# Optimization experiments

Measured on AMD Instinct MI355X. Metric: run time of the kernel, lower is better.

The kernel has to match this reference:

```python
import jax, jax.numpy as jnp
import numpy as np

B, N, C, H = 2, 2048, 768, 12
D = C // H
SCALE = D ** -0.5
STEP = 0.1
LAMBD = 0.5
EPS = 1e-12  # F.normalize eps


def setup_inputs() -> dict:
    key = jax.random.key(0)
    k1, k2, k3 = jax.random.split(key, 3)
    x = jax.random.normal(k1, (B, N, C), dtype=jnp.float32)
    Wqkv = jax.random.normal(k2, (3 * C, C), dtype=jnp.float32) * 0.02
    Wproj = jax.random.normal(k3, (C, C), dtype=jnp.float32) * 0.02
    bproj = jnp.zeros((C,), dtype=jnp.float32)
    return {"x": x, "Wqkv": Wqkv, "Wproj": Wproj, "bproj": bproj}


def _l2_normalize(t):
    # matches F.normalize(t, dim=-1): t / max(||t||_2, eps)
    n = jnp.sqrt(jnp.sum(t * t, axis=-1, keepdims=True))
    return t / jnp.maximum(n, EPS)


def reference(x, Wqkv, Wproj, bproj):
    b, n, c = x.shape
    # qkv: [B,N,3C] -> [3,B,H,N,D]
    qkv = (x @ Wqkv.T).reshape(b, n, 3, H, D).transpose(2, 0, 3, 1, 4)
    q, k, v = qkv[0], qkv[1], qkv[2]
    q = _l2_normalize(q)
    k = _l2_normalize(k)
    attn = jnp.einsum('bhnd,bhmd->bhnm', q, k) * SCALE
    x1 = jnp.einsum('bhnm,bhmd->bhnd', attn, v)        # weight @ x
    grad_1 = jnp.einsum('bhnm,bhnd->bhmd', attn, x1)   # weight^T @ x1
    grad_2 = jnp.einsum('bhnm,bhnd->bhmd', attn, v)    # weight^T @ x
    grad_update = STEP * (grad_2 - grad_1) - STEP * LAMBD
    out = jax.nn.relu(v + grad_update)                 # [B,H,N,D]
    out = out.transpose(0, 2, 1, 3).reshape(b, n, c)   # [B,N,C]
    return out @ Wproj.T + bproj
```

## Files before the change

kernel.cpp:

```cpp
#include <hip/hip_runtime.h>
#include <hip/hip_bf16.h>

typedef __attribute__((ext_vector_type(8))) __bf16 bf16x8;
typedef __attribute__((ext_vector_type(4))) float f32x4;

#define HBF __hip_bfloat16

static constexpr float SCALE_C = 0.125f;
static constexpr float STEP_C  = 0.1f;
static constexpr float LAMBD_C = 0.5f;

__device__ __forceinline__ int sane_f(float v) {
    float a = fabsf(v);
    return (a <= 1.0e4f && (a >= 1.0e-6f || v == 0.0f)) ? 1 : 0;
}

__global__ __launch_bounds__(256) void convert_all(const void* __restrict__ x,
                                                   const void* __restrict__ wqkv,
                                                   const void* __restrict__ wproj,
                                                   const void* __restrict__ bproj,
                                                   HBF* __restrict__ xb,
                                                   HBF* __restrict__ wqkvb,
                                                   HBF* __restrict__ wprojb,
                                                   HBF* __restrict__ bprojb,
                                                   int* __restrict__ flag) {
    const int t = threadIdx.x, lane = t & 63;
    const unsigned int w = ((const unsigned int*)x)[lane];
    const float f  = __uint_as_float(w);
    const float h0 = __uint_as_float((w & 0xFFFFu) << 16);
    const float h1 = __uint_as_float(w & 0xFFFF0000u);
    int s32 = sane_f(f);
    int s16 = sane_f(h0) + sane_f(h1);
#pragma unroll
    for (int off = 32; off >= 1; off >>= 1) {
        s32 += __shfl_xor(s32, off, 64);
        s16 += __shfl_xor(s16, off, 64);
    }
    const int isf32 = (2 * s32 >= s16) ? 1 : 0;
    if (blockIdx.x == 0 && t == 0) flag[0] = isf32;

    constexpr int C0 = (4096 * 768) / 8;
    constexpr int C1 = C0 + (2304 * 768) / 8;
    constexpr int C2 = C1 + (768 * 768) / 8;
    constexpr int C3 = C2 + 768 / 8;

    int i = blockIdx.x * 256 + t;
    const int stride = gridDim.x * 256;
    for (; i < C3; i += stride) {
        const void* src; HBF* dst; int e;
        if (i < C0)      { src = x;     dst = xb;     e = i; }
        else if (i < C1) { src = wqkv;  dst = wqkvb;  e = i - C0; }
        else if (i < C2) { src = wproj; dst = wprojb; e = i - C1; }
        else             { src = bproj; dst = bprojb; e = i - C2; }
        if (isf32) {
            const float4* s = (const float4*)src;
            float4 a = s[2 * e], b = s[2 * e + 1];
            HBF o[8] = {__float2bfloat16(a.x), __float2bfloat16(a.y),
                        __float2bfloat16(a.z), __float2bfloat16(a.w),
                        __float2bfloat16(b.x), __float2bfloat16(b.y),
                        __float2bfloat16(b.z), __float2bfloat16(b.w)};
            ((uint4*)dst)[e] = *(const uint4*)o;
        } else {
            ((uint4*)dst)[e] = ((const uint4*)src)[e];
        }
    }
}

template <int NJ, bool BIAS, bool FINAL, bool SPLITQKV>
__global__ __launch_bounds__(256) void gemm128(const HBF* __restrict__ A,
                                               const HBF* __restrict__ B,
                                               const HBF* __restrict__ bias,
                                               void* __restrict__ Cout,
                                               HBF* __restrict__ qraw,
                                               HBF* __restrict__ vbuf,
                                               int M, int N, int K,
                                               const int* __restrict__ flagp) {
    constexpr int TN = NJ * 32;
    __shared__ HBF smem[128 * 64 + TN * 64];
    HBF* As = smem;
    HBF* Bs = smem + 128 * 64;

    int outf32 = 0;
    if (FINAL) outf32 = *flagp;

    const int tid  = threadIdx.x;
    const int wv   = tid >> 6, lane = tid & 63;
    const int m0   = blockIdx.x * 128, n0 = blockIdx.y * TN;
    const int wr = wv >> 1, wc = wv & 1;
    const int l15 = lane & 15, quad = lane >> 4;
    const int srow   = lane >> 3;
    const int schunk = (lane & 7) ^ srow;

    f32x4 acc[4][NJ] = {};

    for (int k0 = 0; k0 < K; k0 += 64) {
#pragma unroll
        for (int d = 0; d < 4; d++) {
            const int region = d * 4 + wv;
            const int row = region * 8 + srow;
            const HBF* ga = A + (size_t)(m0 + row) * K + k0 + schunk * 8;
            __builtin_amdgcn_global_load_lds((const void*)ga, (void*)(As + region * 512), 16, 0, 0);
        }
#pragma unroll
        for (int d = 0; d < TN / 32; d++) {
            const int region = d * 4 + wv;
            const int row = region * 8 + srow;
            const HBF* gb = B + (size_t)(n0 + row) * K + k0 + schunk * 8;
            __builtin_amdgcn_global_load_lds((const void*)gb, (void*)(Bs + region * 512), 16, 0, 0);
        }
        __syncthreads();

#pragma unroll
        for (int s = 0; s < 2; s++) {
            bf16x8 af[4], bfr[NJ];
#pragma unroll
            for (int i = 0; i < 4; i++) {
                const int row = wr * 64 + i * 16 + l15;
                const int ch = (s * 4 + quad) ^ (row & 7);
                af[i] = *reinterpret_cast<const bf16x8*>(&As[row * 64 + ch * 8]);
            }
#pragma unroll
            for (int j = 0; j < NJ; j++) {
                const int col = wc * (NJ * 16) + j * 16 + l15;
                const int ch = (s * 4 + quad) ^ (col & 7);
                bfr[j] = *reinterpret_cast<const bf16x8*>(&Bs[col * 64 + ch * 8]);
            }
#pragma unroll
            for (int i = 0; i < 4; i++)
#pragma unroll
                for (int j = 0; j < NJ; j++)
                    acc[i][j] = __builtin_amdgcn_mfma_f32_16x16x32_bf16(af[i], bfr[j], acc[i][j], 0, 0, 0);
        }
        __syncthreads();
    }

    float bvals[NJ];
#pragma unroll
    for (int j = 0; j < NJ; j++) {
        bvals[j] = 0.f;
        if (BIAS) bvals[j] = __bfloat162float(bias[n0 + wc * NJ * 16 + j * 16 + l15]);
    }

    if (FINAL && outf32) {
#pragma unroll
        for (int i = 0; i < 4; i++)
#pragma unroll
            for (int j = 0; j < NJ; j++) {
                const int col = n0 + wc * NJ * 16 + j * 16 + l15;
#pragma unroll
                for (int r = 0; r < 4; r++) {
                    const int row = m0 + wr * 64 + i * 16 + quad * 4 + r;
                    ((float*)Cout)[(size_t)row * N + col] = acc[i][j][r] + bvals[j];
                }
            }
        return;
    }

    constexpr int RS = (NJ == 4) ? 72 : 40;
    constexpr int CH = NJ * 2;
    constexpr int ITERS = 32 * CH / 64;
    HBF* ep = smem + wv * (32 * RS);

#pragma unroll
    for (int ih = 0; ih < 2; ih++) {
        __syncthreads();
#pragma unroll
        for (int ii = 0; ii < 2; ii++) {
            const int i = ih * 2 + ii;
#pragma unroll
            for (int j = 0; j < NJ; j++)
#pragma unroll
                for (int r = 0; r < 4; r++)
                    ep[(ii * 16 + quad * 4 + r) * RS + j * 16 + l15] =
                        __float2bfloat16(acc[i][j][r] + bvals[j]);
        }
        __syncthreads();
        const int rowstart = m0 + wr * 64 + ih * 32;
#pragma unroll
        for (int it = 0; it < ITERS; it++) {
            const int idx = it * 64 + lane;
            const int rl = idx / CH, ch = idx % CH;
            const uint4 val = *(const uint4*)((const char*)ep + rl * (RS * 2) + ch * 16);
            if (SPLITQKV) {
                const int colbase = n0 + wc * 64;
                const int tsel = (colbase >= 1536) ? 2 : (colbase >= 768 ? 1 : 0);
                const int h = (colbase - tsel * 768) >> 6;
                HBF* tp = (tsel == 2) ? vbuf : (qraw + (size_t)tsel * (24 * 2048 * 64));
                const int b = rowstart >> 11, n = rowstart & 2047;
                char* dst = (char*)(tp + ((size_t)(b * 12 + h) * 2048 + n) * 64);
                *(uint4*)(dst + rl * 128 + ch * 16) = val;
            } else {
                const int grow = rowstart + rl;
                const int col = n0 + wc * NJ * 16 + ch * 8;
                *(uint4*)((HBF*)Cout + (size_t)grow * N + col) = val;
            }
        }
    }
}

__global__ __launch_bounds__(256) void gram_partial(const HBF* __restrict__ Qraw,
                                                    const HBF* __restrict__ Kraw,
                                                    const HBF* __restrict__ Vb,
                                                    float* __restrict__ P) {
    const int bh = blockIdx.x;
    const int cn = blockIdx.y;
    const int t = threadIdx.x;
    __shared__ float Qs[2048], Ks[2048], Vs[2048];
    const int ti = t >> 4, tj = t & 15;

    float akv[4][4] = {}, aqv[4][4] = {}, aqq[4][4] = {};

    for (int it = 0; it < 2; it++) {
        const size_t gbase = ((size_t)bh * 2048 + cn * 64 + it * 32) * 64 + t * 8;
        __syncthreads();
        {
            uint4 rq = *(const uint4*)(Qraw + gbase);
            uint4 rk = *(const uint4*)(Kraw + gbase);
            uint4 rv = *(const uint4*)(Vb + gbase);
            const HBF* hq = (const HBF*)&rq;
            const HBF* hk = (const HBF*)&rk;
            const HBF* hv = (const HBF*)&rv;
            float q[8], k[8];
            float sq = 0.f, sk = 0.f;
#pragma unroll
            for (int i = 0; i < 8; i++) {
                q[i] = __bfloat162float(hq[i]); sq += q[i] * q[i];
                k[i] = __bfloat162float(hk[i]); sk += k[i] * k[i];
            }
#pragma unroll
            for (int off = 1; off <= 4; off <<= 1) {
                sq += __shfl_xor(sq, off, 64);
                sk += __shfl_xor(sk, off, 64);
            }
            const float iq = 1.0f / fmaxf(sqrtf(sq), 1e-12f);
            const float ik = 1.0f / fmaxf(sqrtf(sk), 1e-12f);
#pragma unroll
            for (int i = 0; i < 8; i++) {
                Qs[t * 8 + i] = q[i] * iq;
                Ks[t * 8 + i] = k[i] * ik;
                Vs[t * 8 + i] = __bfloat162float(hv[i]);
            }
        }
        __syncthreads();

#pragma unroll 4
        for (int nn = 0; nn < 32; nn++) {
            float qi[4], ki[4], vj[4], qj[4];
#pragma unroll
            for (int a = 0; a < 4; a++) {
                qi[a] = Qs[nn * 64 + ti + 16 * a];
                ki[a] = Ks[nn * 64 + ti + 16 * a];
                vj[a] = Vs[nn * 64 + tj + 16 * a];
                qj[a] = Qs[nn * 64 + tj + 16 * a];
            }
#pragma unroll
            for (int a = 0; a < 4; a++)
#pragma unroll
                for (int c = 0; c < 4; c++) {
                    akv[a][c] += ki[a] * vj[c];
                    aqv[a][c] += qi[a] * vj[c];
                    aqq[a][c] += qi[a] * qj[c];
                }
        }
    }

    float* Pb = P + ((size_t)bh * 32 + cn) * 12288;
#pragma unroll
    for (int a = 0; a < 4; a++)
#pragma unroll
        for (int c = 0; c < 4; c++) {
            const int i = ti + 16 * a, j = tj + 16 * c;
            Pb[i * 64 + j]        = akv[a][c];
            Pb[4096 + i * 64 + j] = aqv[a][c];
            Pb[8192 + i * 64 + j] = aqq[a][c];
        }
}

__global__ __launch_bounds__(256) void gram_reduce(const float* __restrict__ P,
                                                   float* __restrict__ M) {
    const int o = blockIdx.x * 256 + threadIdx.x;
    const int head = o / 12288, e = o % 12288;
    const float* Pb = P + (size_t)head * 32 * 12288 + e;
    float s = 0.f;
#pragma unroll
    for (int k = 0; k < 32; k++) s += Pb[(size_t)k * 12288];
    M[o] = s;
}

__global__ __launch_bounds__(256) void combine_w(const float* __restrict__ M,
                                                 HBF* __restrict__ Wt) {
    const int bh = blockIdx.x;
    const int by = blockIdx.y;
    const int t = threadIdx.x;
    __shared__ float Kv[4096];
    __shared__ float Qq8[512];
    const float* Mb = M + (size_t)bh * 12288;
#pragma unroll
    for (int r = 0; r < 16; r++) Kv[t + 256 * r] = Mb[t + 256 * r];
#pragma unroll
    for (int r = 0; r < 2; r++)  Qq8[t + 256 * r] = Mb[8192 + by * 512 + t + 256 * r];
    __syncthreads();

    const int il = t >> 5;
    const int j0 = (t & 31) * 2;
    float s0 = 0.f, s1 = 0.f;
#pragma unroll
    for (int k = 0; k < 64; k++) {
        const float q = Qq8[il * 64 + k];
        const float2 kv = *(const float2*)&Kv[k * 64 + j0];
        s0 += q * kv.x;
        s1 += q * kv.y;
    }
    const int i = by * 8 + il;
    const float w0 = STEP_C * (SCALE_C * Mb[4096 + i * 64 + j0]     - SCALE_C * SCALE_C * s0);
    const float w1 = STEP_C * (SCALE_C * Mb[4096 + i * 64 + j0 + 1] - SCALE_C * SCALE_C * s1);
    Wt[(size_t)bh * 4096 + j0 * 64 + i]       = __float2bfloat16(w0);
    Wt[(size_t)bh * 4096 + (j0 + 1) * 64 + i] = __float2bfloat16(w1);
}

__global__ __launch_bounds__(256) void epilogue_attn(const HBF* __restrict__ Kraw,
                                                     const HBF* __restrict__ Vb,
                                                     const HBF* __restrict__ Wt,
                                                     HBF* __restrict__ AO) {
    __shared__ char smem[34816];
    HBF* Ks  = (HBF*)smem;
    HBF* Wts = Ks + 128 * 64;
    float* Ps = (float*)smem;

    const int bh = blockIdx.x, cn = blockIdx.y;
    const int b = bh / 12, h = bh % 12;
    const int t = threadIdx.x, wv = t >> 6, lane = t & 63;
    const int l15 = lane & 15, quad = lane >> 4;
    const size_t kbase = ((size_t)bh * 2048 + cn * 128) * 64;
    const int sub = t & 7;

#pragma unroll
    for (int rr = 0; rr < 4; rr++) {
        const int row = rr * 32 + (t >> 3);
        uint4 rk = *(const uint4*)(Kraw + kbase + (size_t)row * 64 + sub * 8);
        const HBF* hk = (const HBF*)&rk;
        float k[8]; float sk = 0.f;
#pragma unroll
        for (int i = 0; i < 8; i++) { k[i] = __bfloat162float(hk[i]); sk += k[i] * k[i]; }
#pragma unroll
        for (int off = 1; off <= 4; off <<= 1) sk += __shfl_xor(sk, off, 64);
        const float ik = 1.0f / fmaxf(sqrtf(sk), 1e-12f);
        HBF o[8];
#pragma unroll
        for (int i = 0; i < 8; i++) o[i] = __float2bfloat16(k[i] * ik);
        const int ch = sub ^ (row & 7);
        *(uint4*)(Ks + row * 64 + ch * 8) = *(const uint4*)o;
    }
#pragma unroll
    for (int rr = 0; rr < 2; rr++) {
        const int d = rr * 32 + (t >> 3);
        uint4 v = *(const uint4*)(Wt + (size_t)bh * 4096 + d * 64 + sub * 8);
        const int ch = sub ^ (d & 7);
        *(uint4*)(Wts + d * 64 + ch * 8) = v;
    }
    __syncthreads();

    f32x4 acc[2][4] = {};
#pragma unroll
    for (int s = 0; s < 2; s++) {
        bf16x8 af[2], bfr[4];
#pragma unroll
        for (int i = 0; i < 2; i++) {
            const int row = wv * 32 + i * 16 + l15;
            const int ch = (s * 4 + quad) ^ (row & 7);
            af[i] = *reinterpret_cast<const bf16x8*>(&Ks[row * 64 + ch * 8]);
        }
#pragma unroll
        for (int j = 0; j < 4; j++) {
            const int d = j * 16 + l15;
            const int ch = (s * 4 + quad) ^ (d & 7);
            bfr[j] = *reinterpret_cast<const bf16x8*>(&Wts[d * 64 + ch * 8]);
        }
#pragma unroll
        for (int i = 0; i < 2; i++)
#pragma unroll
            for (int j = 0; j < 4; j++)
                acc[i][j] = __builtin_amdgcn_mfma_f32_16x16x32_bf16(af[i], bfr[j], acc[i][j], 0, 0, 0);
    }
    __syncthreads();

    float* Pw = Ps + wv * (32 * 68);
#pragma unroll
    for (int i = 0; i < 2; i++)
#pragma unroll
        for (int j = 0; j < 4; j++)
#pragma unroll
            for (int r = 0; r < 4; r++)
                Pw[(i * 16 + quad * 4 + r) * 68 + j * 16 + l15] = acc[i][j][r];
    __syncthreads();

#pragma unroll
    for (int rr = 0; rr < 4; rr++) {
        const int row = rr * 32 + (t >> 3);
        const float* prow = Ps + (row >> 5) * (32 * 68) + (row & 31) * 68 + sub * 8;
        const float4 p0 = *(const float4*)prow;
        const float4 p1 = *(const float4*)(prow + 4);
        uint4 rv = *(const uint4*)(Vb + kbase + (size_t)row * 64 + sub * 8);
        const HBF* hv = (const HBF*)&rv;
        const float pv[8] = {p0.x, p0.y, p0.z, p0.w, p1.x, p1.y, p1.z, p1.w};
        HBF o[8];
#pragma unroll
        for (int i = 0; i < 8; i++)
            o[i] = __float2bfloat16(fmaxf(__bfloat162float(hv[i]) + pv[i] - (STEP_C * LAMBD_C), 0.f));
        const int n = cn * 128 + row;
        *(uint4*)(AO + ((size_t)b * 2048 + n) * 768 + h * 64 + sub * 8) = *(const uint4*)o;
    }
}

extern "C" void kernel_launch(void* const* d_in, const int* in_sizes, int n_in,
                              void* d_out, int out_size, void* d_ws, size_t ws_size,
                              hipStream_t stream) {
    char* ws = (char*)d_ws;
    size_t off = 0;
    int*   flag   = (int*)(ws + off);   off += 16;
    HBF*   xb     = (HBF*)(ws + off);   off += (size_t)4096 * 768 * 2;
    HBF*   Wqkvb  = (HBF*)(ws + off);   off += (size_t)2304 * 768 * 2;
    HBF*   Wprojb = (HBF*)(ws + off);   off += (size_t)768 * 768 * 2;
    HBF*   bprojb = (HBF*)(ws + off);   off += 2048;
    HBF*   QKraw  = (HBF*)(ws + off);   off += (size_t)2 * 24 * 2048 * 64 * 2;
    HBF*   Vb     = (HBF*)(ws + off);   off += (size_t)24 * 2048 * 64 * 2;
    float* P      = (float*)(ws + off); off += (size_t)24 * 32 * 12288 * 4;
    float* M      = (float*)(ws + off); off += (size_t)24 * 12288 * 4;
    HBF*   Wt     = (HBF*)(ws + off);   off += (size_t)24 * 4096 * 2;
    HBF*   AO     = (HBF*)(ws + off);   off += (size_t)4096 * 768 * 2;

    HBF* Qraw = QKraw;
    HBF* Kraw = QKraw + (size_t)24 * 2048 * 64;

    convert_all<<<2048, 256, 0, stream>>>(d_in[0], d_in[1], d_in[2], d_in[3],
                                          xb, Wqkvb, Wprojb, bprojb, flag);

    gemm128<4, false, false, true><<<dim3(32, 18), 256, 0, stream>>>(
        xb, Wqkvb, nullptr, nullptr, QKraw, Vb, 4096, 2304, 768, nullptr);

    gram_partial<<<dim3(24, 32), 256, 0, stream>>>(Qraw, Kraw, Vb, P);
    gram_reduce<<<1152, 256, 0, stream>>>(P, M);

    combine_w<<<dim3(24, 8), 256, 0, stream>>>(M, Wt);

    epilogue_attn<<<dim3(24, 16), 256, 0, stream>>>(Kraw, Vb, Wt, AO);

    gemm128<2, true, true, false><<<dim3(32, 12), 256, 0, stream>>>(
        AO, Wprojb, bprojb, d_out, nullptr, nullptr, 4096, 768, 768, flag);
}
```

Before: 155.9 us.

## Fuse L2-normalize into QKV GEMM epilogue and compute Gram matrices with MFMA

```diff
diff --git a/kernel.cpp b/kernel.cpp
--- a/kernel.cpp
+++ b/kernel.cpp
@@ -71,8 +71,9 @@
                                                const HBF* __restrict__ B,
                                                const HBF* __restrict__ bias,
                                                void* __restrict__ Cout,
-                                               HBF* __restrict__ qraw,
-                                               HBF* __restrict__ vbuf,
+                                               HBF* __restrict__ knat,
+                                               HBF* __restrict__ vnat,
+                                               HBF* __restrict__ tbuf,
                                                int M, int N, int K,
                                                const int* __restrict__ flagp) {
     constexpr int TN = NJ * 32;
@@ -134,6 +135,79 @@
         __syncthreads();
     }
 
+    if (SPLITQKV) {
+        HBF* wpriv = smem + wv * 4096;
+        const int colbase = n0 + wc * 64;
+        const int tsel = (colbase >= 1536) ? 2 : (colbase >= 768 ? 1 : 0);
+        const int h = (colbase - tsel * 768) >> 6;
+
+        if (tsel < 2) {
+#pragma unroll
+            for (int i = 0; i < 4; i++)
+#pragma unroll
+                for (int r = 0; r < 4; r++) {
+                    float ss = acc[i][0][r] * acc[i][0][r] + acc[i][1][r] * acc[i][1][r]
+                             + acc[i][2][r] * acc[i][2][r] + acc[i][3][r] * acc[i][3][r];
+#pragma unroll
+                    for (int off = 1; off <= 8; off <<= 1) ss += __shfl_xor(ss, off, 64);
+                    const float inv = 1.0f / fmaxf(sqrtf(ss), 1e-12f);
+#pragma unroll
+                    for (int j = 0; j < 4; j++) acc[i][j][r] *= inv;
+                }
+        }
+
+#pragma unroll
+        for (int ih = 0; ih < 2; ih++) {
+            const int rowstart = m0 + wr * 64 + ih * 32;
+            const int b = rowstart >> 11, nloc = rowstart & 2047;
+            const size_t bh = (size_t)(b * 12 + h);
+
+            if (tsel != 0) {
+                HBF* ep = wpriv;
+#pragma unroll
+                for (int ii = 0; ii < 2; ii++) {
+                    const int i = ih * 2 + ii;
+#pragma unroll
+                    for (int j = 0; j < 4; j++)
+#pragma unroll
+                        for (int r = 0; r < 4; r++)
+                            ep[(ii * 16 + quad * 4 + r) * 72 + j * 16 + l15] =
+                                __float2bfloat16(acc[i][j][r]);
+                }
+                HBF* dst0 = ((tsel == 2) ? vnat : knat) + (bh * 2048 + nloc) * 64;
+#pragma unroll
+                for (int it = 0; it < 4; it++) {
+                    const int idx = it * 64 + lane;
+                    const int rl = idx >> 3, ch = idx & 7;
+                    const uint4 val = *(const uint4*)((const char*)ep + rl * 144 + ch * 16);
+                    *(uint4*)((char*)dst0 + rl * 128 + ch * 16) = val;
+                }
+            }
+            {
+                HBF* epT = wpriv;
+#pragma unroll
+                for (int ii = 0; ii < 2; ii++) {
+                    const int i = ih * 2 + ii;
+#pragma unroll
+                    for (int j = 0; j < 4; j++)
+#pragma unroll
+                        for (int r = 0; r < 4; r++)
+                            epT[(j * 16 + l15) * 34 + ii * 16 + quad * 4 + r] =
+                                __float2bfloat16(acc[i][j][r]);
+                }
+                HBF* tdst = tbuf + (size_t)tsel * (24 * 64 * 2048) + (bh * 64) * 2048 + nloc;
+#pragma unroll
+                for (int it = 0; it < 4; it++) {
+                    const int idx = it * 64 + lane;
+                    const int d = idx >> 2, c = idx & 3;
+                    const uint4 val = *(const uint4*)(epT + d * 34 + c * 8);
+                    *(uint4*)(tdst + (size_t)d * 2048 + c * 8) = val;
+                }
+            }
+        }
+        return;
+    }
+
     float bvals[NJ];
 #pragma unroll
     for (int j = 0; j < NJ; j++) {
@@ -163,7 +237,6 @@
 
 #pragma unroll
     for (int ih = 0; ih < 2; ih++) {
-        __syncthreads();
 #pragma unroll
         for (int ii = 0; ii < 2; ii++) {
             const int i = ih * 2 + ii;
@@ -174,105 +247,73 @@
                     ep[(ii * 16 + quad * 4 + r) * RS + j * 16 + l15] =
                         __float2bfloat16(acc[i][j][r] + bvals[j]);
         }
-        __syncthreads();
         const int rowstart = m0 + wr * 64 + ih * 32;
 #pragma unroll
         for (int it = 0; it < ITERS; it++) {
             const int idx = it * 64 + lane;
             const int rl = idx / CH, ch = idx % CH;
             const uint4 val = *(const uint4*)((const char*)ep + rl * (RS * 2) + ch * 16);
-            if (SPLITQKV) {
-                const int colbase = n0 + wc * 64;
-                const int tsel = (colbase >= 1536) ? 2 : (colbase >= 768 ? 1 : 0);
-                const int h = (colbase - tsel * 768) >> 6;
-                HBF* tp = (tsel == 2) ? vbuf : (qraw + (size_t)tsel * (24 * 2048 * 64));
-                const int b = rowstart >> 11, n = rowstart & 2047;
-                char* dst = (char*)(tp + ((size_t)(b * 12 + h) * 2048 + n) * 64);
-                *(uint4*)(dst + rl * 128 + ch * 16) = val;
-            } else {
-                const int grow = rowstart + rl;
-                const int col = n0 + wc * NJ * 16 + ch * 8;
-                *(uint4*)((HBF*)Cout + (size_t)grow * N + col) = val;
-            }
-        }
-    }
-}
-
-__global__ __launch_bounds__(256) void gram_partial(const HBF* __restrict__ Qraw,
-                                                    const HBF* __restrict__ Kraw,
-                                                    const HBF* __restrict__ Vb,
-                                                    float* __restrict__ P) {
-    const int bh = blockIdx.x;
-    const int cn = blockIdx.y;
-    const int t = threadIdx.x;
-    __shared__ float Qs[2048], Ks[2048], Vs[2048];
-    const int ti = t >> 4, tj = t & 15;
-
-    float akv[4][4] = {}, aqv[4][4] = {}, aqq[4][4] = {};
-
-    for (int it = 0; it < 2; it++) {
-        const size_t gbase = ((size_t)bh * 2048 + cn * 64 + it * 32) * 64 + t * 8;
-        __syncthreads();
-        {
-            uint4 rq = *(const uint4*)(Qraw + gbase);
-            uint4 rk = *(const uint4*)(Kraw + gbase);
-            uint4 rv = *(const uint4*)(Vb + gbase);
-            const HBF* hq = (const HBF*)&rq;
-            const HBF* hk = (const HBF*)&rk;
-            const HBF* hv = (const HBF*)&rv;
-            float q[8], k[8];
-            float sq = 0.f, sk = 0.f;
-#pragma unroll
-            for (int i = 0; i < 8; i++) {
-                q[i] = __bfloat162float(hq[i]); sq += q[i] * q[i];
-                k[i] = __bfloat162float(hk[i]); sk += k[i] * k[i];
-            }
-#pragma unroll
-            for (int off = 1; off <= 4; off <<= 1) {
-                sq += __shfl_xor(sq, off, 64);
-                sk += __shfl_xor(sk, off, 64);
-            }
-            const float iq = 1.0f / fmaxf(sqrtf(sq), 1e-12f);
-            const float ik = 1.0f / fmaxf(sqrtf(sk), 1e-12f);
-#pragma unroll
-            for (int i = 0; i < 8; i++) {
-                Qs[t * 8 + i] = q[i] * iq;
-                Ks[t * 8 + i] = k[i] * ik;
-                Vs[t * 8 + i] = __bfloat162float(hv[i]);
-            }
-        }
-        __syncthreads();
-
-#pragma unroll 4
-        for (int nn = 0; nn < 32; nn++) {
-            float qi[4], ki[4], vj[4], qj[4];
-#pragma unroll
-            for (int a = 0; a < 4; a++) {
-                qi[a] = Qs[nn * 64 + ti + 16 * a];
-                ki[a] = Ks[nn * 64 + ti + 16 * a];
-                vj[a] = Vs[nn * 64 + tj + 16 * a];
-                qj[a] = Qs[nn * 64 + tj + 16 * a];
-            }
-#pragma unroll
-            for (int a = 0; a < 4; a++)
-#pragma unroll
-                for (int c = 0; c < 4; c++) {
-                    akv[a][c] += ki[a] * vj[c];
-                    aqv[a][c] += qi[a] * vj[c];
-                    aqq[a][c] += qi[a] * qj[c];
-                }
-        }
-    }
-
-    float* Pb = P + ((size_t)bh * 32 + cn) * 12288;
-#pragma unroll
-    for (int a = 0; a < 4; a++)
-#pragma unroll
-        for (int c = 0; c < 4; c++) {
-            const int i = ti + 16 * a, j = tj + 16 * c;
-            Pb[i * 64 + j]        = akv[a][c];
-            Pb[4096 + i * 64 + j] = aqv[a][c];
-            Pb[8192 + i * 64 + j] = aqq[a][c];
+            const int grow = rowstart + rl;
+            const int col = n0 + wc * NJ * 16 + ch * 8;
+            *(uint4*)((HBF*)Cout + (size_t)grow * N + col) = val;
+        }
+    }
+}
+
+__global__ __launch_bounds__(256) void gram_mfma(const HBF* __restrict__ QKVt,
+                                                 float* __restrict__ P) {
+    __shared__ HBF lds[3 * 8192];
+    const int bh = blockIdx.x, cn = blockIdx.y;
+    const int t = threadIdx.x, wv = t >> 6, lane = t & 63;
+    const int l15 = lane & 15, quad = lane >> 4;
+    constexpr size_t S = (size_t)24 * 64 * 2048;
+    const HBF* srcs[3] = {QKVt + S, QKVt, QKVt + 2 * S};
+
+    const int rowq = lane >> 4;
+    const int cgb  = lane & 15;
+#pragma unroll
+    for (int t3 = 0; t3 < 3; t3++) {
+        const HBF* base = srcs[t3] + (size_t)bh * 64 * 2048 + cn * 128;
+#pragma unroll
+        for (int rg = 0; rg < 4; rg++) {
+            const int region = rg * 4 + wv;
+            const int row = region * 4 + rowq;
+            const int cg = cgb ^ (row & 15);
+            __builtin_amdgcn_global_load_lds((const void*)(base + (size_t)row * 2048 + cg * 8),
+                                             (void*)(lds + t3 * 8192 + region * 512), 16, 0, 0);
+        }
+    }
+    __syncthreads();
+
+    const HBF* Kt = lds;
+    const HBF* Qt = lds + 8192;
+    const HBF* Vt = lds + 16384;
+    f32x4 aKV[4] = {}, aQV[4] = {}, aQQ[4] = {};
+    const int i = wv;
+#pragma unroll
+    for (int s = 0; s < 4; s++) {
+        const int q = (s * 4 + quad) ^ l15;
+        const bf16x8 aK = *(const bf16x8*)(Kt + (i * 16 + l15) * 128 + q * 8);
+        const bf16x8 aQ = *(const bf16x8*)(Qt + (i * 16 + l15) * 128 + q * 8);
+#pragma unroll
+        for (int j = 0; j < 4; j++) {
+            const bf16x8 bV = *(const bf16x8*)(Vt + (j * 16 + l15) * 128 + q * 8);
+            const bf16x8 bQ = *(const bf16x8*)(Qt + (j * 16 + l15) * 128 + q * 8);
+            aKV[j] = __builtin_amdgcn_mfma_f32_16x16x32_bf16(aK, bV, aKV[j], 0, 0, 0);
+            aQV[j] = __builtin_amdgcn_mfma_f32_16x16x32_bf16(aQ, bV, aQV[j], 0, 0, 0);
+            aQQ[j] = __builtin_amdgcn_mfma_f32_16x16x32_bf16(aQ, bQ, aQQ[j], 0, 0, 0);
+        }
+    }
+
+    float* Pb = P + ((size_t)bh * 16 + cn) * 12288;
+#pragma unroll
+    for (int j = 0; j < 4; j++)
+#pragma unroll
+        for (int r = 0; r < 4; r++) {
+            const int row = i * 16 + quad * 4 + r, col = j * 16 + l15;
+            Pb[row * 64 + col]        = aKV[j][r];
+            Pb[4096 + row * 64 + col] = aQV[j][r];
+            Pb[8192 + row * 64 + col] = aQQ[j][r];
         }
 }
 
@@ -280,10 +321,10 @@
                                                    float* __restrict__ M) {
     const int o = blockIdx.x * 256 + threadIdx.x;
     const int head = o / 12288, e = o % 12288;
-    const float* Pb = P + (size_t)head * 32 * 12288 + e;
+    const float* Pb = P + (size_t)head * 16 * 12288 + e;
     float s = 0.f;
 #pragma unroll
-    for (int k = 0; k < 32; k++) s += Pb[(size_t)k * 12288];
+    for (int k = 0; k < 16; k++) s += Pb[(size_t)k * 12288];
     M[o] = s;
 }
 
@@ -318,7 +359,7 @@
     Wt[(size_t)bh * 4096 + (j0 + 1) * 64 + i] = __float2bfloat16(w1);
 }
 
-__global__ __launch_bounds__(256) void epilogue_attn(const HBF* __restrict__ Kraw,
+__global__ __launch_bounds__(256) void epilogue_attn(const HBF* __restrict__ Kn,
                                                      const HBF* __restrict__ Vb,
                                                      const HBF* __restrict__ Wt,
                                                      HBF* __restrict__ AO) {
@@ -332,48 +373,39 @@
     const int t = threadIdx.x, wv = t >> 6, lane = t & 63;
     const int l15 = lane & 15, quad = lane >> 4;
     const size_t kbase = ((size_t)bh * 2048 + cn * 128) * 64;
+    const int srow = lane >> 3;
+    const int schunk = (lane & 7) ^ srow;
     const int sub = t & 7;
 
 #pragma unroll
-    for (int rr = 0; rr < 4; rr++) {
-        const int row = rr * 32 + (t >> 3);
-        uint4 rk = *(const uint4*)(Kraw + kbase + (size_t)row * 64 + sub * 8);
-        const HBF* hk = (const HBF*)&rk;
-        float k[8]; float sk = 0.f;
-#pragma unroll
-        for (int i = 0; i < 8; i++) { k[i] = __bfloat162float(hk[i]); sk += k[i] * k[i]; }
-#pragma unroll
-        for (int off = 1; off <= 4; off <<= 1) sk += __shfl_xor(sk, off, 64);
-        const float ik = 1.0f / fmaxf(sqrtf(sk), 1e-12f);
-        HBF o[8];
-#pragma unroll
-        for (int i = 0; i < 8; i++) o[i] = __float2bfloat16(k[i] * ik);
-        const int ch = sub ^ (row & 7);
-        *(uint4*)(Ks + row * 64 + ch * 8) = *(const uint4*)o;
-    }
-#pragma unroll
-    for (int rr = 0; rr < 2; rr++) {
-        const int d = rr * 32 + (t >> 3);
-        uint4 v = *(const uint4*)(Wt + (size_t)bh * 4096 + d * 64 + sub * 8);
-        const int ch = sub ^ (d & 7);
-        *(uint4*)(Wts + d * 64 + ch * 8) = v;
+    for (int rg = 0; rg < 4; rg++) {
+        const int region = rg * 4 + wv;
+        const int row = region * 8 + srow;
+        __builtin_amdgcn_global_load_lds((const void*)(Kn + kbase + (size_t)row * 64 + schunk * 8),
+                                         (void*)(Ks + region * 512), 16, 0, 0);
+    }
+#pragma unroll
+    for (int rg = 0; rg < 2; rg++) {
+        const int region = rg * 4 + wv;
+        const int row = region * 8 + srow;
+        __builtin_amdgcn_global_load_lds((const void*)(Wt + (size_t)bh * 4096 + (size_t)row * 64 + schunk * 8),
+                                         (void*)(Wts + region * 512), 16, 0, 0);
     }
     __syncthreads();
 
     f32x4 acc[2][4] = {};
 #pragma unroll
     for (int s = 0; s < 2; s++) {
+        const int ch = (s * 4 + quad) ^ (l15 & 7);
         bf16x8 af[2], bfr[4];
 #pragma unroll
         for (int i = 0; i < 2; i++) {
             const int row = wv * 32 + i * 16 + l15;
-            const int ch = (s * 4 + quad) ^ (row & 7);
             af[i] = *reinterpret_cast<const bf16x8*>(&Ks[row * 64 + ch * 8]);
         }
 #pragma unroll
         for (int j = 0; j < 4; j++) {
             const int d = j * 16 + l15;
-            const int ch = (s * 4 + quad) ^ (d & 7);
             bfr[j] = *reinterpret_cast<const bf16x8*>(&Wts[d * 64 + ch * 8]);
         }
 #pragma unroll
@@ -422,29 +454,27 @@
     HBF*   Wqkvb  = (HBF*)(ws + off);   off += (size_t)2304 * 768 * 2;
     HBF*   Wprojb = (HBF*)(ws + off);   off += (size_t)768 * 768 * 2;
     HBF*   bprojb = (HBF*)(ws + off);   off += 2048;
-    HBF*   QKraw  = (HBF*)(ws + off);   off += (size_t)2 * 24 * 2048 * 64 * 2;
+    HBF*   Kn     = (HBF*)(ws + off);   off += (size_t)24 * 2048 * 64 * 2;
     HBF*   Vb     = (HBF*)(ws + off);   off += (size_t)24 * 2048 * 64 * 2;
-    float* P      = (float*)(ws + off); off += (size_t)24 * 32 * 12288 * 4;
+    HBF*   QKVt   = (HBF*)(ws + off);   off += (size_t)3 * 24 * 64 * 2048 * 2;
+    float* P      = (float*)(ws + off); off += (size_t)24 * 16 * 12288 * 4;
     float* M      = (float*)(ws + off); off += (size_t)24 * 12288 * 4;
     HBF*   Wt     = (HBF*)(ws + off);   off += (size_t)24 * 4096 * 2;
     HBF*   AO     = (HBF*)(ws + off);   off += (size_t)4096 * 768 * 2;
 
-    HBF* Qraw = QKraw;
-    HBF* Kraw = QKraw + (size_t)24 * 2048 * 64;
-
     convert_all<<<2048, 256, 0, stream>>>(d_in[0], d_in[1], d_in[2], d_in[3],
                                           xb, Wqkvb, Wprojb, bprojb, flag);
 
     gemm128<4, false, false, true><<<dim3(32, 18), 256, 0, stream>>>(
-        xb, Wqkvb, nullptr, nullptr, QKraw, Vb, 4096, 2304, 768, nullptr);
-
-    gram_partial<<<dim3(24, 32), 256, 0, stream>>>(Qraw, Kraw, Vb, P);
+        xb, Wqkvb, nullptr, nullptr, Kn, Vb, QKVt, 4096, 2304, 768, nullptr);
+
+    gram_mfma<<<dim3(24, 16), 256, 0, stream>>>(QKVt, P);
     gram_reduce<<<1152, 256, 0, stream>>>(P, M);
 
     combine_w<<<dim3(24, 8), 256, 0, stream>>>(M, Wt);
 
-    epilogue_attn<<<dim3(24, 16), 256, 0, stream>>>(Kraw, Vb, Wt, AO);
+    epilogue_attn<<<dim3(24, 16), 256, 0, stream>>>(Kn, Vb, Wt, AO);
 
     gemm128<2, true, true, false><<<dim3(32, 12), 256, 0, stream>>>(
-        AO, Wprojb, bprojb, d_out, nullptr, nullptr, 4096, 768, 768, flag);
-}
+        AO, Wprojb, bprojb, d_out, nullptr, nullptr, nullptr, 4096, 768, 768, flag);
+}
```

After: 153.5 us. About the same (-1.6%).
